# Optimization experiments

Measured on AMD Instinct MI355X. Metric: run time of the kernel, lower is better.

The kernel has to match this reference:

```python
import jax, jax.numpy as jnp
import numpy as np


def setup_inputs() -> dict:
    key = jax.random.key(0)
    ks = jax.random.split(key, 10)
    B, S, I, Hy, H = 16, 4096, 256, 64, 512
    sc = 0.05
    return {
        "x": jax.random.normal(ks[0], (B, S, I), jnp.float32),
        "hidden": jax.random.normal(ks[1], (B, H), jnp.float32),
        "lin0_W": jax.random.normal(ks[2], (Hy, I), jnp.float32) * sc,
        "lin0_b": jax.random.normal(ks[3], (Hy,), jnp.float32) * sc,
        "sig0_W": jax.random.normal(ks[4], (Hy, I), jnp.float32) * sc,
        "sig0_b": jax.random.normal(ks[5], (Hy,), jnp.float32) * sc,
        "fch_W": jax.random.normal(ks[6], (H, Hy), jnp.float32) * sc,
        "fch_b": jax.random.normal(ks[7], (H,), jnp.float32) * sc,
        "fc2_W": jax.random.normal(ks[8], (H, I), jnp.float32) * sc,
        "fc2_b": jax.random.normal(ks[9], (H,), jnp.float32) * sc,
    }


def reference(x, hidden, lin0_W, lin0_b, sig0_W, sig0_b, fch_W, fch_b, fc2_W, fc2_b):
    # GLN sub-network (num_layers=1): relu(linear(x) * sigmoid(linear(x)))
    lin = jnp.einsum('bsi,hi->bsh', x, lin0_W) + lin0_b          # [B,S,Hy]
    gate = jax.nn.sigmoid(jnp.einsum('bsi,hi->bsh', x, sig0_W) + sig0_b)
    g = jax.nn.relu(lin * gate)                                   # [B,S,Hy]
    b = jnp.einsum('bsh,dh->bsd', g, fch_W) + fch_b               # [B,S,H]
    # multihead gating
    sig_alphas = jax.nn.sigmoid(jnp.einsum('bsi,di->bsd', x, fc2_W) + fc2_b)
    b = b * sig_alphas

    # sequential recurrence: h_t = relu(b_t + roll(h_{t-1}, 1, -1)); h_{-1} = hidden
    def step(h, b_t):
        h = jax.nn.relu(b_t + jnp.roll(h, 1, axis=-1))
        return h, h

    b_tmajor = jnp.swapaxes(b, 0, 1)  # [S,B,H]
    last, outs = jax.lax.scan(step, hidden, b_tmajor)
    outputs = jnp.swapaxes(outs, 0, 1)  # [B,S,H]
    return outputs, last
```

## Files before the change

### kernel.cpp

```cpp
#include <hip/hip_runtime.h>

typedef __attribute__((ext_vector_type(4))) float  f32x4;
typedef __attribute__((ext_vector_type(4))) short  s16x4;
typedef __attribute__((ext_vector_type(8))) short  s16x8;
typedef __bf16 bf16x8 __attribute__((ext_vector_type(8)));

#define NBATCH 16
#define SEQ    4096
#define KIN    256
#define HY     64
#define HOUT   512
#define NROWS  (NBATCH*SEQ)
#define LC     32
#define NC     (SEQ/LC)

#define GP(x) ((const __attribute__((address_space(1))) void*)(x))
#define LP(x) ((__attribute__((address_space(3))) void*)(x))

static __device__ __forceinline__ short f2bf(float f) {
  unsigned u = __float_as_uint(f);
  u = u + 0x7FFF + ((u >> 16) & 1);
  return (short)(u >> 16);
}
static __device__ __forceinline__ float bf2f(short h) {
  return __uint_as_float(((unsigned)(unsigned short)h) << 16);
}
static __device__ __forceinline__ f32x4 mfma16(bf16x8 a, bf16x8 b, f32x4 c) {
  return __builtin_amdgcn_mfma_f32_16x16x32_bf16(a, b, c, 0, 0, 0);
}
static __device__ __forceinline__ bf16x8 ldfrag(const short* p) {
  return *reinterpret_cast<const bf16x8*>(p);
}
static __device__ __forceinline__ float fsigmoid(float z) {
  return 1.f / (1.f + __expf(-z));
}

__global__ void prep_w(const float* __restrict__ lin0W, const float* __restrict__ sig0W,
                       const float* __restrict__ fchW,  const float* __restrict__ fc2W,
                       short* __restrict__ W1h, short* __restrict__ W2h,
                       short* __restrict__ Fh,  short* __restrict__ F2h) {
  int i = blockIdx.x * 256 + threadIdx.x;
  if (i < 16384) {
    W1h[i] = f2bf(lin0W[i]);
    W2h[i] = f2bf(sig0W[i]);
  } else if (i < 16384 + 32768) {
    Fh[i - 16384] = f2bf(fchW[i - 16384]);
  } else if (i < 16384 + 32768 + 131072) {
    F2h[i - 49152] = f2bf(fc2W[i - 49152]);
  }
}

__global__ __launch_bounds__(256) void gx(
    const float* __restrict__ x,
    const short* __restrict__ W1h, const short* __restrict__ W2h,
    const float* __restrict__ lin0b, const float* __restrict__ sig0b,
    short* __restrict__ Gh, short* __restrict__ xh) {
  __shared__ __align__(16) short smem[64 * 256 + 64 * 64];
  short* Ah = smem;
  short* gL = smem + 64 * 256;
  int tid = threadIdx.x;
  int row0 = blockIdx.x * 64;
  #pragma unroll
  for (int i = 0; i < 16; ++i) {
    int f4 = tid + i * 256;
    int r = f4 >> 6, k = (f4 & 63) << 2;
    f32x4 v = *reinterpret_cast<const f32x4*>(x + (size_t)(row0 + r) * KIN + k);
    s16x4 hh;
    #pragma unroll
    for (int j = 0; j < 4; ++j) hh[j] = f2bf(v[j]);
    *reinterpret_cast<s16x4*>(&Ah[(r * 256 + k) ^ ((r & 7) << 3)]) = hh;
    *reinterpret_cast<s16x4*>(xh + (size_t)(row0 + r) * KIN + k) = hh;
  }
  __syncthreads();
  int w = tid >> 6, l = tid & 63, lr = l & 15, lg = l >> 4;
  {
    int c = w * 16 + lr;
    f32x4 a1[4], a2[4];
    #pragma unroll
    for (int rt = 0; rt < 4; ++rt) { a1[rt] = (f32x4)0.f; a2[rt] = (f32x4)0.f; }
    #pragma unroll
    for (int ks = 0; ks < 8; ++ks) {
      int kk = ks * 32 + lg * 8;
      bf16x8 b1 = ldfrag(W1h + c * 256 + kk);
      bf16x8 b2 = ldfrag(W2h + c * 256 + kk);
      #pragma unroll
      for (int rt = 0; rt < 4; ++rt) {
        int r = rt * 16 + lr;
        bf16x8 a = ldfrag(&Ah[(r * 256 + kk) ^ ((r & 7) << 3)]);
        a1[rt] = mfma16(b1, a, a1[rt]);
        a2[rt] = mfma16(b2, a, a2[rt]);
      }
    }
    f32x4 blv = *reinterpret_cast<const f32x4*>(lin0b + w * 16 + lg * 4);
    f32x4 bsv = *reinterpret_cast<const f32x4*>(sig0b + w * 16 + lg * 4);
    #pragma unroll
    for (int rt = 0; rt < 4; ++rt) {
      int xrl = rt * 16 + lr;
      s16x4 gg;
      #pragma unroll
      for (int j = 0; j < 4; ++j) {
        float g = (a1[rt][j] + blv[j]) * fsigmoid(a2[rt][j] + bsv[j]);
        gg[j] = f2bf(g > 0.f ? g : 0.f);
      }
      *reinterpret_cast<s16x4*>(&gL[(xrl * 64 + w * 16 + lg * 4) ^ ((xrl & 7) << 3)]) = gg;
    }
  }
  __syncthreads();
  #pragma unroll
  for (int i = 0; i < 2; ++i) {
    int slot = i * 256 + tid;
    int row = slot >> 3, c8 = slot & 7;
    s16x8 v = *reinterpret_cast<const s16x8*>(&gL[(row * 64 + c8 * 8) ^ ((row & 7) << 3)]);
    *reinterpret_cast<s16x8*>(Gh + (size_t)(row0 + row) * HY + c8 * 8) = v;
  }
}

__global__ __launch_bounds__(512, 4) void bg(
    const short* __restrict__ xh, const short* __restrict__ Gh,
    const short* __restrict__ F2h, const short* __restrict__ Fh,
    const float* __restrict__ fchb, const float* __restrict__ fc2b,
    short* __restrict__ Bb) {
  __shared__ __align__(16) short smem[2][16384];
  short* bT = &smem[0][0];
  int tid = threadIdx.x;
  int w = tid >> 6, l = tid & 63;
  int lr = l & 15, lg = l >> 4;
  int r0 = (w >> 1) * 32;
  int c0 = (w & 1) * 64;
  int bid = blockIdx.x;
  int v = (bid & 7) * 256 + (bid >> 3);
  int rowTile = v & 511;
  int colTile = v >> 9;
  int row0 = rowTile * 128;
  int col0 = colTile * 128;

  auto stage = [&](int t, int b) {
    short* As = &smem[b][0];
    short* Bs = &smem[b][8192];
    #pragma unroll
    for (int j = 0; j < 1; ++j) {
    }
    #pragma unroll
    for (int j = 0; j < 2; ++j) {
      int blk = w * 2 + j;
      int flat = blk * 64 + l;
      int row = flat >> 3, sp = flat & 7;
      int seg = sp ^ (row & 7);
      const short* asrc = (t < 4) ? xh + (size_t)(row0 + row) * KIN + t * 64 + seg * 8
                                  : Gh + (size_t)(row0 + row) * HY + seg * 8;
      const short* bsrc = (t < 4) ? F2h + (size_t)(col0 + row) * KIN + t * 64 + seg * 8
                                  : Fh + (size_t)(col0 + row) * HY + seg * 8;
      __builtin_amdgcn_global_load_lds(GP(asrc), LP(&As[blk * 512]), 16, 0, 0);
      __builtin_amdgcn_global_load_lds(GP(bsrc), LP(&Bs[blk * 512]), 16, 0, 0);
    }
  };
  auto compute = [&](int b, f32x4 (&acc)[2][4]) {
    short* As = &smem[b][0];
    short* Bs = &smem[b][8192];
    #pragma unroll
    for (int ksl = 0; ksl < 2; ++ksl) {
      bf16x8 Af[2], Bf[4];
      #pragma unroll
      for (int i = 0; i < 2; ++i) {
        int row = r0 + i * 16 + lr;
        Af[i] = ldfrag(&As[row * 64 + ((ksl * 32 + lg * 8) ^ ((row & 7) << 3))]);
      }
      #pragma unroll
      for (int i = 0; i < 4; ++i) {
        int col = c0 + i * 16 + lr;
        Bf[i] = ldfrag(&Bs[col * 64 + ((ksl * 32 + lg * 8) ^ ((col & 7) << 3))]);
      }
      #pragma unroll
      for (int rt = 0; rt < 2; ++rt)
        #pragma unroll
        for (int ct = 0; ct < 4; ++ct)
          acc[rt][ct] = mfma16(Af[rt], Bf[ct], acc[rt][ct]);
    }
  };

  f32x4 acc2[2][4], accF[2][4];
  #pragma unroll
  for (int rt = 0; rt < 2; ++rt)
    #pragma unroll
    for (int ct = 0; ct < 4; ++ct) { acc2[rt][ct] = (f32x4)0.f; accF[rt][ct] = (f32x4)0.f; }

  stage(0, 0);
  __syncthreads();
  #pragma unroll
  for (int t = 0; t < 5; ++t) {
    if (t < 4) stage(t + 1, (t + 1) & 1);
    if (t < 4) compute(t & 1, acc2);
    else       compute(t & 1, accF);
    __syncthreads();
  }

  #pragma unroll
  for (int ct = 0; ct < 4; ++ct) {
    int lc = c0 + ct * 16 + lr;
    int col = col0 + lc;
    float bc = fchb[col], b2c = fc2b[col];
    #pragma unroll
    for (int rt = 0; rt < 2; ++rt) {
      int tl0 = r0 + rt * 16 + lg * 4;
      #pragma unroll
      for (int j = 0; j < 4; ++j) {
        int tl = tl0 + j;
        float alpha = fsigmoid(acc2[rt][ct][j] + b2c);
        bT[(tl * 128 + lc) ^ ((tl & 7) << 3)] = f2bf((accF[rt][ct][j] + bc) * alpha);
      }
    }
  }
  __syncthreads();
  #pragma unroll
  for (int i = 0; i < 4; ++i) {
    int slot = i * 512 + tid;
    int row = slot >> 4, c8 = slot & 15;
    s16x8 vv = *reinterpret_cast<const s16x8*>(&bT[(row * 128 + c8 * 8) ^ ((row & 7) << 3)]);
    *reinterpret_cast<s16x8*>(Bb + (size_t)(row0 + row) * HOUT + col0 + c8 * 8) = vv;
  }
}

__global__ __launch_bounds__(64) void scan_passA(const short* __restrict__ Bb,
                                                 float* __restrict__ Cc, float* __restrict__ Sc) {
  int bc = blockIdx.x;
  int l = threadIdx.x;
  int row0 = bc * LC;
  const short* bp = Bb + (size_t)row0 * HOUT + l * 8;
  s16x8 vc = *reinterpret_cast<const s16x8*>(bp);
  float C[8], S[8];
  #pragma unroll
  for (int i = 0; i < 8; ++i) { S[i] = bf2f(vc[i]); C[i] = 0.f; }
  for (int t = 1; t < LC; ++t) {
    s16x8 vn = *reinterpret_cast<const s16x8*>(bp + (size_t)t * HOUT);
    float bb[8];
    #pragma unroll
    for (int i = 0; i < 8; ++i) bb[i] = bf2f(vn[i]);
    float pC = __shfl(C[7], (l + 63) & 63);
    float pS = __shfl(S[7], (l + 63) & 63);
    #pragma unroll
    for (int i = 7; i >= 1; --i) { C[i] = fmaxf(0.f, bb[i] + C[i - 1]); S[i] = bb[i] + S[i - 1]; }
    C[0] = fmaxf(0.f, bb[0] + pC);
    S[0] = bb[0] + pS;
  }
  float* cp = Cc + (size_t)bc * HOUT + l * 8;
  float* sp = Sc + (size_t)bc * HOUT + l * 8;
  #pragma unroll
  for (int i = 0; i < 8; ++i) { cp[i] = C[i]; sp[i] = S[i]; }
}

__global__ __launch_bounds__(64) void scan_combine(const float* __restrict__ hidden,
                                                   const float* __restrict__ Cc, const float* __restrict__ Sc,
                                                   float* __restrict__ hIn, float* __restrict__ lastOut) {
  int batch = blockIdx.x;
  int l = threadIdx.x;
  float h[8];
  const float* hp = hidden + batch * HOUT + l * 8;
  #pragma unroll
  for (int i = 0; i < 8; ++i) h[i] = hp[i];
  size_t base0 = ((size_t)batch * NC) * HOUT + l * 8;
  f32x4 c0 = *reinterpret_cast<const f32x4*>(Cc + base0);
  f32x4 c1 = *reinterpret_cast<const f32x4*>(Cc + base0 + 4);
  f32x4 s0 = *reinterpret_cast<const f32x4*>(Sc + base0);
  f32x4 s1 = *reinterpret_cast<const f32x4*>(Sc + base0 + 4);
  for (int c = 0; c < NC; ++c) {
    size_t base = base0 + (size_t)c * HOUT;
    f32x4 nc0, nc1, ns0, ns1;
    if (c + 1 < NC) {
      size_t nb = base + HOUT;
      nc0 = *reinterpret_cast<const f32x4*>(Cc + nb);
      nc1 = *reinterpret_cast<const f32x4*>(Cc + nb + 4);
      ns0 = *reinterpret_cast<const f32x4*>(Sc + nb);
      ns1 = *reinterpret_cast<const f32x4*>(Sc + nb + 4);
    }
    #pragma unroll
    for (int i = 0; i < 8; ++i) hIn[base + i] = h[i];
    float hs[8];
    #pragma unroll
    for (int i = 0; i < 8; ++i) hs[i] = __shfl(h[i], (l + 64 - (LC / 8)) & 63);
    #pragma unroll
    for (int i = 0; i < 4; ++i) {
      h[i]     = fmaxf(c0[i], s0[i] + hs[i]);
      h[4 + i] = fmaxf(c1[i], s1[i] + hs[4 + i]);
    }
    c0 = nc0; c1 = nc1; s0 = ns0; s1 = ns1;
  }
  float* lp = lastOut + batch * HOUT + l * 8;
  #pragma unroll
  for (int i = 0; i < 8; ++i) lp[i] = h[i];
}

__global__ __launch_bounds__(64) void scan_passB(const short* __restrict__ bws,
                                                 const float* __restrict__ hIn,
                                                 float* __restrict__ hout) {
  int bc = blockIdx.x;
  int l = threadIdx.x;
  int row0 = bc * LC;
  const float* hp = hIn + (size_t)bc * HOUT + l * 8;
  float h[8];
  #pragma unroll
  for (int i = 0; i < 8; ++i) h[i] = hp[i];
  s16x8 vc = *reinterpret_cast<const s16x8*>(bws + (size_t)row0 * HOUT + l * 8);
  for (int t = 0; t < LC; ++t) {
    s16x8 vn;
    if (t + 1 < LC)
      vn = *reinterpret_cast<const s16x8*>(bws + (size_t)(row0 + t + 1) * HOUT + l * 8);
    float bb[8];
    #pragma unroll
    for (int i = 0; i < 8; ++i) bb[i] = bf2f(vc[i]);
    float ph = __shfl(h[7], (l + 63) & 63);
    #pragma unroll
    for (int i = 7; i >= 1; --i) h[i] = fmaxf(0.f, bb[i] + h[i - 1]);
    h[0] = fmaxf(0.f, bb[0] + ph);
    f32x4 o0, o1;
    #pragma unroll
    for (int i = 0; i < 4; ++i) { o0[i] = h[i]; o1[i] = h[4 + i]; }
    float* bt = hout + (size_t)(row0 + t) * HOUT + l * 8;
    *reinterpret_cast<f32x4*>(bt) = o0;
    *reinterpret_cast<f32x4*>(bt + 4) = o1;
    vc = vn;
  }
}

extern "C" void kernel_launch(void* const* d_in, const int* in_sizes, int n_in,
                              void* d_out, int out_size, void* d_ws, size_t ws_size,
                              hipStream_t stream) {
  (void)in_sizes; (void)n_in; (void)out_size; (void)ws_size;
  const float* x      = (const float*)d_in[0];
  const float* hidden = (const float*)d_in[1];
  const float* lin0W  = (const float*)d_in[2];
  const float* lin0b  = (const float*)d_in[3];
  const float* sig0W  = (const float*)d_in[4];
  const float* sig0b  = (const float*)d_in[5];
  const float* fchW   = (const float*)d_in[6];
  const float* fchb   = (const float*)d_in[7];
  const float* fc2W   = (const float*)d_in[8];
  const float* fc2b   = (const float*)d_in[9];
  float* outO  = (float*)d_out;
  float* lastO = outO + (size_t)NROWS * HOUT;

  char* wsb = (char*)d_ws;
  size_t off = 0;
  auto alloc = [&](size_t bytes) { char* p = wsb + off; off += (bytes + 255) & ~(size_t)255; return p; };
  float* Cc  = (float*)alloc((size_t)NBATCH * NC * HOUT * 4);
  float* Sc  = (float*)alloc((size_t)NBATCH * NC * HOUT * 4);
  float* hIn = (float*)alloc((size_t)NBATCH * NC * HOUT * 4);
  short* W1h = (short*)alloc(HY * KIN * 2);
  short* W2h = (short*)alloc(HY * KIN * 2);
  short* Fh  = (short*)alloc(HOUT * HY * 2);
  short* F2h = (short*)alloc(HOUT * KIN * 2);
  short* Gh  = (short*)alloc((size_t)NROWS * HY * 2);
  short* xh  = (short*)alloc((size_t)NROWS * KIN * 2);
  short* Bb  = (short*)alloc((size_t)NROWS * HOUT * 2);

  prep_w<<<704, 256, 0, stream>>>(lin0W, sig0W, fchW, fc2W, W1h, W2h, Fh, F2h);
  gx<<<NROWS / 64, 256, 0, stream>>>(x, W1h, W2h, lin0b, sig0b, Gh, xh);
  bg<<<2048, 512, 0, stream>>>(xh, Gh, F2h, Fh, fchb, fc2b, Bb);
  scan_passA<<<NBATCH * NC, 64, 0, stream>>>(Bb, Cc, Sc);
  scan_combine<<<NBATCH, 64, 0, stream>>>(hidden, Cc, Sc, hIn, lastO);
  scan_passB<<<NBATCH * NC, 64, 0, stream>>>(Bb, hIn, outO);
}
```

Baseline: 178.7 us.

## Widen x conversion loads, remap bg tiles per XCD, deepen scan prefetching

```diff
diff --git a/kernel.cpp b/kernel.cpp
--- a/kernel.cpp
+++ b/kernel.cpp
@@ -61,15 +61,17 @@
   int tid = threadIdx.x;
   int row0 = blockIdx.x * 64;
   #pragma unroll
-  for (int i = 0; i < 16; ++i) {
-    int f4 = tid + i * 256;
-    int r = f4 >> 6, k = (f4 & 63) << 2;
-    f32x4 v = *reinterpret_cast<const f32x4*>(x + (size_t)(row0 + r) * KIN + k);
-    s16x4 hh;
-    #pragma unroll
-    for (int j = 0; j < 4; ++j) hh[j] = f2bf(v[j]);
-    *reinterpret_cast<s16x4*>(&Ah[(r * 256 + k) ^ ((r & 7) << 3)]) = hh;
-    *reinterpret_cast<s16x4*>(xh + (size_t)(row0 + r) * KIN + k) = hh;
+  for (int i = 0; i < 8; ++i) {
+    int slot = i * 256 + tid;
+    int r = slot >> 5, k8 = slot & 31;
+    const float* xp = x + (size_t)(row0 + r) * KIN + k8 * 8;
+    f32x4 v0 = *reinterpret_cast<const f32x4*>(xp);
+    f32x4 v1 = *reinterpret_cast<const f32x4*>(xp + 4);
+    s16x8 hh;
+    #pragma unroll
+    for (int j = 0; j < 4; ++j) { hh[j] = f2bf(v0[j]); hh[4 + j] = f2bf(v1[j]); }
+    *reinterpret_cast<s16x8*>(&Ah[(r * 256 + k8 * 8) ^ ((r & 7) << 3)]) = hh;
+    *reinterpret_cast<s16x8*>(xh + (size_t)(row0 + r) * KIN + k8 * 8) = hh;
   }
   __syncthreads();
   int w = tid >> 6, l = tid & 63, lr = l & 15, lg = l >> 4;
@@ -128,18 +130,15 @@
   int r0 = (w >> 1) * 32;
   int c0 = (w & 1) * 64;
   int bid = blockIdx.x;
-  int v = (bid & 7) * 256 + (bid >> 3);
-  int rowTile = v & 511;
-  int colTile = v >> 9;
+  int xcd = bid & 7, idx = bid >> 3;
+  int colTile = xcd >> 1;
+  int rowTile = ((xcd & 1) << 8) + idx;
   int row0 = rowTile * 128;
   int col0 = colTile * 128;
 
   auto stage = [&](int t, int b) {
     short* As = &smem[b][0];
     short* Bs = &smem[b][8192];
-    #pragma unroll
-    for (int j = 0; j < 1; ++j) {
-    }
     #pragma unroll
     for (int j = 0; j < 2; ++j) {
       int blk = w * 2 + j;
@@ -226,21 +225,24 @@
   int l = threadIdx.x;
   int row0 = bc * LC;
   const short* bp = Bb + (size_t)row0 * HOUT + l * 8;
-  s16x8 vc = *reinterpret_cast<const s16x8*>(bp);
+  s16x8 v0 = *reinterpret_cast<const s16x8*>(bp);
   float C[8], S[8];
   #pragma unroll
-  for (int i = 0; i < 8; ++i) { S[i] = bf2f(vc[i]); C[i] = 0.f; }
+  for (int i = 0; i < 8; ++i) { S[i] = bf2f(v0[i]); C[i] = 0.f; }
+  s16x8 vc = *reinterpret_cast<const s16x8*>(bp + (size_t)HOUT);
   for (int t = 1; t < LC; ++t) {
-    s16x8 vn = *reinterpret_cast<const s16x8*>(bp + (size_t)t * HOUT);
+    s16x8 vn;
+    if (t + 1 < LC) vn = *reinterpret_cast<const s16x8*>(bp + (size_t)(t + 1) * HOUT);
     float bb[8];
     #pragma unroll
-    for (int i = 0; i < 8; ++i) bb[i] = bf2f(vn[i]);
+    for (int i = 0; i < 8; ++i) bb[i] = bf2f(vc[i]);
     float pC = __shfl(C[7], (l + 63) & 63);
     float pS = __shfl(S[7], (l + 63) & 63);
     #pragma unroll
     for (int i = 7; i >= 1; --i) { C[i] = fmaxf(0.f, bb[i] + C[i - 1]); S[i] = bb[i] + S[i - 1]; }
     C[0] = fmaxf(0.f, bb[0] + pC);
     S[0] = bb[0] + pS;
+    vc = vn;
   }
   float* cp = Cc + (size_t)bc * HOUT + l * 8;
   float* sp = Sc + (size_t)bc * HOUT + l * 8;
@@ -258,31 +260,41 @@
   #pragma unroll
   for (int i = 0; i < 8; ++i) h[i] = hp[i];
   size_t base0 = ((size_t)batch * NC) * HOUT + l * 8;
-  f32x4 c0 = *reinterpret_cast<const f32x4*>(Cc + base0);
-  f32x4 c1 = *reinterpret_cast<const f32x4*>(Cc + base0 + 4);
-  f32x4 s0 = *reinterpret_cast<const f32x4*>(Sc + base0);
-  f32x4 s1 = *reinterpret_cast<const f32x4*>(Sc + base0 + 4);
-  for (int c = 0; c < NC; ++c) {
-    size_t base = base0 + (size_t)c * HOUT;
-    f32x4 nc0, nc1, ns0, ns1;
-    if (c + 1 < NC) {
-      size_t nb = base + HOUT;
-      nc0 = *reinterpret_cast<const f32x4*>(Cc + nb);
-      nc1 = *reinterpret_cast<const f32x4*>(Cc + nb + 4);
-      ns0 = *reinterpret_cast<const f32x4*>(Sc + nb);
-      ns1 = *reinterpret_cast<const f32x4*>(Sc + nb + 4);
-    }
-    #pragma unroll
-    for (int i = 0; i < 8; ++i) hIn[base + i] = h[i];
-    float hs[8];
-    #pragma unroll
-    for (int i = 0; i < 8; ++i) hs[i] = __shfl(h[i], (l + 64 - (LC / 8)) & 63);
-    #pragma unroll
-    for (int i = 0; i < 4; ++i) {
-      h[i]     = fmaxf(c0[i], s0[i] + hs[i]);
-      h[4 + i] = fmaxf(c1[i], s1[i] + hs[4 + i]);
-    }
-    c0 = nc0; c1 = nc1; s0 = ns0; s1 = ns1;
+  f32x4 pc0[4], pc1[4], ps0[4], ps1[4];
+  #pragma unroll
+  for (int s = 0; s < 4; ++s) {
+    size_t b = base0 + (size_t)s * HOUT;
+    pc0[s] = *reinterpret_cast<const f32x4*>(Cc + b);
+    pc1[s] = *reinterpret_cast<const f32x4*>(Cc + b + 4);
+    ps0[s] = *reinterpret_cast<const f32x4*>(Sc + b);
+    ps1[s] = *reinterpret_cast<const f32x4*>(Sc + b + 4);
+  }
+  for (int cg = 0; cg < NC; cg += 4) {
+    #pragma unroll
+    for (int s = 0; s < 4; ++s) {
+      int c = cg + s;
+      size_t base = base0 + (size_t)c * HOUT;
+      f32x4 h0, h1;
+      #pragma unroll
+      for (int i = 0; i < 4; ++i) { h0[i] = h[i]; h1[i] = h[4 + i]; }
+      *reinterpret_cast<f32x4*>(hIn + base) = h0;
+      *reinterpret_cast<f32x4*>(hIn + base + 4) = h1;
+      float hs[8];
+      #pragma unroll
+      for (int i = 0; i < 8; ++i) hs[i] = __shfl(h[i], (l + 60) & 63);
+      #pragma unroll
+      for (int i = 0; i < 4; ++i) {
+        h[i]     = fmaxf(pc0[s][i], ps0[s][i] + hs[i]);
+        h[4 + i] = fmaxf(pc1[s][i], ps1[s][i] + hs[4 + i]);
+      }
+      if (c + 4 < NC) {
+        size_t nb = base + (size_t)4 * HOUT;
+        pc0[s] = *reinterpret_cast<const f32x4*>(Cc + nb);
+        pc1[s] = *reinterpret_cast<const f32x4*>(Cc + nb + 4);
+        ps0[s] = *reinterpret_cast<const f32x4*>(Sc + nb);
+        ps1[s] = *reinterpret_cast<const f32x4*>(Sc + nb + 4);
+      }
+    }
   }
   float* lp = lastOut + batch * HOUT + l * 8;
   #pragma unroll
```

Result: faster. 168.8 us (-5.6%).
